# Kernel optimization log

Hardware: AMD Instinct MI355X
Metric: run time of the kernel (lower is better)

## Reference

```python
import jax, jax.numpy as jnp
import numpy as np

B, C, H, W = 32, 64, 64, 64
K, D = 512, 64
COMMITMENT_COST = 0.25


def setup_inputs() -> dict:
    key = jax.random.key(0)
    k1, k2, k3 = jax.random.split(key, 3)
    inputs = jax.random.normal(k1, (B, C, H, W), dtype=jnp.float32)
    codebook0 = jax.random.normal(k2, (K, D), dtype=jnp.float32)
    codebook1 = jax.random.normal(k3, (K, D), dtype=jnp.float32)
    return {"inputs": inputs, "codebook0": codebook0, "codebook1": codebook1, "idx": 1}


def reference(inputs, codebook0, codebook1, idx):
    # NCHW -> NHWC, flatten to [N, D]
    x = jnp.transpose(inputs, (0, 2, 3, 1))
    flat = x.reshape(-1, D)  # [N, D]
    if idx == 0:
        codes = codebook0
    else:
        codes = jnp.concatenate([codebook0, codebook1], axis=0)  # [2K, D]
    # squared-distance matrix [N, 2K]
    distances = (jnp.sum(flat * flat, axis=1, keepdims=True)
                 + jnp.sum(codes * codes, axis=1)
                 - 2.0 * jnp.matmul(flat, codes.T))
    encoding_indices = jnp.argmin(distances, axis=1)  # [N]
    # gather == one-hot @ codes, without materializing one-hot
    quantized = jnp.take(codes, encoding_indices, axis=0).reshape(x.shape)
    sg = jax.lax.stop_gradient
    e_latent_loss = jnp.mean((sg(quantized) - x) ** 2)
    q_latent_loss = jnp.mean((quantized - sg(x)) ** 2)
    loss = q_latent_loss + COMMITMENT_COST * e_latent_loss
    # straight-through estimator
    quantized_st = x + sg(quantized - x)
    # perplexity from usage histogram (== mean of one-hot encodings)
    n = flat.shape[0]
    counts = jnp.zeros((codes.shape[0],), dtype=jnp.float32).at[encoding_indices].add(1.0)
    avg_probs = counts / n
    perplexity = jnp.exp(-jnp.sum(avg_probs * jnp.log(avg_probs + 1e-10)))
    return (jnp.transpose(quantized_st, (0, 3, 1, 2)), loss, perplexity)
```

## Files before the change

kernel.cpp:

```cpp
#include <hip/hip_runtime.h>


typedef __attribute__((ext_vector_type(8))) short short8;
typedef __attribute__((ext_vector_type(16))) float f32x16;

#define LOSS_OFF 0
#define PART_OFF 2048
#define PACKED_OFF 34816
#define NPART 32
#define CHUNK_B 24576

#define GLL16(gsrc, ldst)                                                      \
  __builtin_amdgcn_global_load_lds(                                            \
      (const __attribute__((address_space(1))) void*)(gsrc),                   \
      (__attribute__((address_space(3))) void*)(ldst), 16, 0, 0)

__device__ __forceinline__ unsigned short bf16_rne(float v, float& rest) {
  const unsigned u = __float_as_uint(v);
  const unsigned r = u + 0x7fffu + ((u >> 16) & 1u);
  const unsigned short h = (unsigned short)(r >> 16);
  rest = v - __uint_as_float((unsigned)h << 16);
  return h;
}

__global__ void vq_pack(const float* __restrict__ cb0, const float* __restrict__ cb1,
                        float* __restrict__ ws) {
  const int c = blockIdx.x * 256 + threadIdx.x;
  if (c < NPART) ws[LOSS_OFF + c] = 0.0f;
#pragma unroll
  for (int p = 0; p < NPART; ++p) ws[PART_OFF + p * 1024 + c] = 0.0f;
  const float* row = (c < 512) ? (cb0 + (size_t)c * 64) : (cb1 + (size_t)(c - 512) * 64);
  float v[64];
  float nrm = 0.f;
#pragma unroll
  for (int d = 0; d < 64; d += 4) {
    const float4 f = *(const float4*)(row + d);
    v[d] = f.x; v[d + 1] = f.y; v[d + 2] = f.z; v[d + 3] = f.w;
    nrm += f.x * f.x + f.y * f.y + f.z * f.z + f.w * f.w;
  }
  unsigned short hi[64], lo[64];
#pragma unroll
  for (int d = 0; d < 64; ++d) {
    float rest, dump;
    hi[d] = bf16_rne(v[d], rest);
    lo[d] = bf16_rne(rest, dump);
  }
  float* base = ws + PACKED_OFF + (size_t)(c >> 6) * 6144 + (c & 63) * 4;
#pragma unroll
  for (int g = 0; g < 16; ++g) {
    short8 gr;
#pragma unroll
    for (int e = 0; e < 8; ++e)
      gr[e] = (short)((g < 8) ? hi[g * 8 + e] : lo[(g - 8) * 8 + e]);
    *(short8*)(base + g * 256) = gr;
  }
  {
    const float nh = -0.5f * nrm;
    float r1, r2, dump;
    const unsigned short n0 = bf16_rne(nh, r1);
    const unsigned short n1 = bf16_rne(r1, r2);
    const unsigned short n2 = bf16_rne(r2, dump);
    short8 g16 = {(short)n0, (short)n1, (short)n2, 0, 0, 0, 0, 0};
    *(short8*)(base + 16 * 256) = g16;
    short8 zz = {0, 0, 0, 0, 0, 0, 0, 0};
    *(short8*)(base + 17 * 256) = zz;
  }
}

__global__ __launch_bounds__(256, 2) void vq_dist(
    const float* __restrict__ xin, const int* __restrict__ idxp,
    const float* __restrict__ cb0, const float* __restrict__ cb1,
    float* __restrict__ out, float* __restrict__ ws) {
  __shared__ char ring[73728];
  const int tid = threadIdx.x;
  const int w = tid >> 6;
  const int l = tid & 63;
  const int half = l >> 5;
  const int col = l & 31;
  const int blk = blockIdx.x;
  const int bb = blk >> 4;
  const int hw0 = (blk & 15) << 8;
  const int nch = (*idxp == 0) ? 8 : 16;
  const char* pk = (const char*)(ws + PACKED_OFF);

  auto stage = [&](int ch, int buf) {
    const char* src = pk + (size_t)ch * CHUNK_B + w * 6144 + l * 16;
    char* dst = ring + buf * CHUNK_B + w * 6144;
#pragma unroll
    for (int i = 0; i < 6; ++i) GLL16(src + i * 1024, dst + i * 1024);
  };
  stage(0, 0);
  stage(1, 1);

  short8 xh[2][4], xl[2][4];
  float xx[2];
#pragma unroll
  for (int m = 0; m < 2; ++m) {
    float vv[4][8];
    const float* xb =
        xin + ((size_t)(bb * 64 + half * 8)) * 4096 + hw0 + w * 64 + m * 32 + col;
#pragma unroll
    for (int kf = 0; kf < 4; ++kf)
#pragma unroll
      for (int j = 0; j < 8; ++j)
        vv[kf][j] = xb[((size_t)(kf * 16 + j)) * 4096];
    float s = 0.f;
#pragma unroll
    for (int kf = 0; kf < 4; ++kf)
#pragma unroll
      for (int j = 0; j < 8; ++j) {
        const float v = vv[kf][j];
        float rest, dump;
        xh[m][kf][j] = (short)bf16_rne(v, rest);
        xl[m][kf][j] = (short)bf16_rne(rest, dump);
        s += v * v;
      }
    s += __shfl_xor(s, 32);
    xx[m] = s;
  }
  short8 xnh;
#pragma unroll
  for (int j = 0; j < 8; ++j)
    xnh[j] = (short)((half == 0 && j < 3) ? 0x3F80 : 0);
  const f32x16 ZV = (f32x16)0.0f;

  float best[2][16];
#pragma unroll
  for (int m = 0; m < 2; ++m)
#pragma unroll
    for (int r = 0; r < 16; ++r) best[m][r] = -3.4e38f;

  for (int i = 0; i < nch; ++i) {
    if (i < nch - 1) {
      asm volatile("s_waitcnt vmcnt(6)" ::: "memory");
    } else {
      asm volatile("s_waitcnt vmcnt(0)" ::: "memory");
    }
    __builtin_amdgcn_s_barrier();
    if (i + 2 < nch) stage(i + 2, (i + 2) % 3);
    const char* bufp = ring + (i % 3) * CHUNK_B;
    const char* tb0 = bufp + col * 16;
    const char* tb1 = bufp + (32 + col) * 16;

    __builtin_amdgcn_s_setprio(1);
    const short8 An0 = *(const short8*)(tb0 + (16 + half) * 1024);
    const short8 An1 = *(const short8*)(tb1 + (16 + half) * 1024);
    f32x16 a00 = __builtin_amdgcn_mfma_f32_32x32x16_bf16(An0, xnh, ZV, 0, 0, 0);
    f32x16 a01 = __builtin_amdgcn_mfma_f32_32x32x16_bf16(An1, xnh, ZV, 0, 0, 0);
    f32x16 a10 = __builtin_amdgcn_mfma_f32_32x32x16_bf16(An0, xnh, ZV, 0, 0, 0);
    f32x16 a11 = __builtin_amdgcn_mfma_f32_32x32x16_bf16(An1, xnh, ZV, 0, 0, 0);
#pragma unroll
    for (int kf = 0; kf < 4; ++kf) {
      const short8 Ah0 = *(const short8*)(tb0 + (2 * kf + half) * 1024);
      const short8 Ah1 = *(const short8*)(tb1 + (2 * kf + half) * 1024);
      const short8 Al0 = *(const short8*)(tb0 + (8 + 2 * kf + half) * 1024);
      const short8 Al1 = *(const short8*)(tb1 + (8 + 2 * kf + half) * 1024);
      a00 = __builtin_amdgcn_mfma_f32_32x32x16_bf16(Ah0, xh[0][kf], a00, 0, 0, 0);
      a01 = __builtin_amdgcn_mfma_f32_32x32x16_bf16(Ah1, xh[0][kf], a01, 0, 0, 0);
      a10 = __builtin_amdgcn_mfma_f32_32x32x16_bf16(Ah0, xh[1][kf], a10, 0, 0, 0);
      a11 = __builtin_amdgcn_mfma_f32_32x32x16_bf16(Ah1, xh[1][kf], a11, 0, 0, 0);
      a00 = __builtin_amdgcn_mfma_f32_32x32x16_bf16(Ah0, xl[0][kf], a00, 0, 0, 0);
      a01 = __builtin_amdgcn_mfma_f32_32x32x16_bf16(Ah1, xl[0][kf], a01, 0, 0, 0);
      a10 = __builtin_amdgcn_mfma_f32_32x32x16_bf16(Ah0, xl[1][kf], a10, 0, 0, 0);
      a11 = __builtin_amdgcn_mfma_f32_32x32x16_bf16(Ah1, xl[1][kf], a11, 0, 0, 0);
      a00 = __builtin_amdgcn_mfma_f32_32x32x16_bf16(Al0, xh[0][kf], a00, 0, 0, 0);
      a01 = __builtin_amdgcn_mfma_f32_32x32x16_bf16(Al1, xh[0][kf], a01, 0, 0, 0);
      a10 = __builtin_amdgcn_mfma_f32_32x32x16_bf16(Al0, xh[1][kf], a10, 0, 0, 0);
      a11 = __builtin_amdgcn_mfma_f32_32x32x16_bf16(Al1, xh[1][kf], a11, 0, 0, 0);
    }
    __builtin_amdgcn_s_setprio(0);

    const unsigned sid0 = (unsigned)(31 - 2 * i);
    const unsigned sid1 = (unsigned)(30 - 2 * i);
#pragma unroll
    for (int r = 0; r < 16; ++r) {
      const float p00 = __uint_as_float((__float_as_uint(a00[r]) & 0xFFFFFFE0u) | sid0);
      const float p01 = __uint_as_float((__float_as_uint(a01[r]) & 0xFFFFFFE0u) | sid1);
      best[0][r] = fmaxf(fmaxf(p00, p01), best[0][r]);
      const float p10 = __uint_as_float((__float_as_uint(a10[r]) & 0xFFFFFFE0u) | sid0);
      const float p11 = __uint_as_float((__float_as_uint(a11[r]) & 0xFFFFFFE0u) | sid1);
      best[1][r] = fmaxf(fmaxf(p10, p11), best[1][r]);
    }
  }

  __syncthreads();
  int* qidxL = (int*)ring;

  float ls = 0.f;
#pragma unroll
  for (int m = 0; m < 2; ++m) {
    float win = best[m][0];
    int wr = 0;
#pragma unroll
    for (int r = 1; r < 16; ++r) {
      const bool g = best[m][r] > win;
      win = g ? best[m][r] : win;
      wr = g ? r : wr;
    }
    const unsigned u = __float_as_uint(win);
    const int t = 31 - (int)(u & 31u);
    int code = (t >> 1) * 64 + (t & 1) * 32 + ((wr & 3) + 8 * (wr >> 2) + 4 * half);
    float clean = __uint_as_float(u & 0xFFFFFFE0u);
    const float ocl = __shfl_xor(clean, 32);
    const int oc = __shfl_xor(code, 32);
    const bool take = (ocl > clean) || (ocl == clean && oc < code);
    clean = take ? ocl : clean;
    code = take ? oc : code;
    if (half == 0) {
      qidxL[w * 64 + m * 32 + col] = code;
      ls += xx[m] - 2.0f * clean;
    }
  }
#pragma unroll
  for (int mk = 1; mk < 64; mk <<= 1) ls += __shfl_xor(ls, mk);
  if (l == 0) atomicAdd(&ws[LOSS_OFF + (blk & (NPART - 1))], ls);
  __syncthreads();

  const int ci = qidxL[tid];
  atomicAdd(ws + PART_OFF + (size_t)(blk & (NPART - 1)) * 1024 + ci, 1.0f);
  const float* crow = (ci < 512) ? (cb0 + (size_t)ci * 64) : (cb1 + (size_t)(ci - 512) * 64);
  float* ob = out + (((size_t)(bb * 64)) << 12) + hw0 + tid;
#pragma unroll
  for (int d4 = 0; d4 < 16; ++d4) {
    const float4 f = *(const float4*)(crow + d4 * 4);
    ob[((size_t)(d4 * 4 + 0)) << 12] = f.x;
    ob[((size_t)(d4 * 4 + 1)) << 12] = f.y;
    ob[((size_t)(d4 * 4 + 2)) << 12] = f.z;
    ob[((size_t)(d4 * 4 + 3)) << 12] = f.w;
  }
}

__global__ void vq_final(const float* __restrict__ ws, float* __restrict__ out) {
  __shared__ float sred[256];
  const int t = threadIdx.x;
  float h = 0.f;
#pragma unroll
  for (int i = t; i < 1024; i += 256) {
    float s = 0.f;
#pragma unroll
    for (int p = 0; p < NPART; ++p) s += ws[PART_OFF + p * 1024 + i];
    const float avg = s * (1.0f / 131072.0f);
    h += avg * logf(avg + 1e-10f);
  }
  sred[t] = h;
  __syncthreads();
  for (int s2 = 128; s2 > 0; s2 >>= 1) {
    if (t < s2) sred[t] += sred[t + s2];
    __syncthreads();
  }
  if (t == 0) {
    float lsum = 0.f;
#pragma unroll
    for (int p = 0; p < NPART; ++p) lsum += ws[LOSS_OFF + p];
    out[8388608] = 1.25f * lsum * (1.0f / 8388608.0f);
    out[8388609] = expf(-sred[0]);
  }
}

extern "C" void kernel_launch(void* const* d_in, const int* in_sizes, int n_in,
                              void* d_out, int out_size, void* d_ws, size_t ws_size,
                              hipStream_t stream) {
  (void)in_sizes; (void)n_in; (void)out_size; (void)ws_size;
  const float* xin = (const float*)d_in[0];
  const float* cb0 = (const float*)d_in[1];
  const float* cb1 = (const float*)d_in[2];
  const int* idxp = (const int*)d_in[3];
  float* out = (float*)d_out;
  float* ws = (float*)d_ws;

  vq_pack<<<4, 256, 0, stream>>>(cb0, cb1, ws);
  vq_dist<<<512, 256, 0, stream>>>(xin, idxp, cb0, cb1, out, ws);
  vq_final<<<1, 256, 0, stream>>>(ws, out);
}
```

Baseline: 77.64 us.

## Read packed codebook directly from global memory instead of LDS ring

Removes the triple-buffered LDS staging of the packed codebook via global_load_lds, along with its barriers and waitcnts. Each wave now loads its codebook fragments straight from global memory, relying on L1/L2 caching, with a 2x unrolled chunk loop. The packed layout is shrunk to drop the unused padding group, and LDS use falls to a small index buffer, which could allow more occupancy. In exchange every wave issues its own global loads with higher latency, and there is no longer an explicit prefetch to hide that latency.

```diff
diff --git a/kernel.cpp b/kernel.cpp
--- a/kernel.cpp
+++ b/kernel.cpp
@@ -8,12 +8,7 @@
 #define PART_OFF 2048
 #define PACKED_OFF 34816
 #define NPART 32
-#define CHUNK_B 24576
-
-#define GLL16(gsrc, ldst)                                                      \
-  __builtin_amdgcn_global_load_lds(                                            \
-      (const __attribute__((address_space(1))) void*)(gsrc),                   \
-      (__attribute__((address_space(3))) void*)(ldst), 16, 0, 0)
+#define CHUNK_B 18432
 
 __device__ __forceinline__ unsigned short bf16_rne(float v, float& rest) {
   const unsigned u = __float_as_uint(v);
@@ -45,7 +40,7 @@
     hi[d] = bf16_rne(v[d], rest);
     lo[d] = bf16_rne(rest, dump);
   }
-  float* base = ws + PACKED_OFF + (size_t)(c >> 6) * 6144 + (c & 63) * 4;
+  float* base = ws + PACKED_OFF + (size_t)(c >> 6) * 4608 + (c & 63) * 4;
 #pragma unroll
   for (int g = 0; g < 16; ++g) {
     short8 gr;
@@ -71,7 +66,7 @@
     const float* __restrict__ xin, const int* __restrict__ idxp,
     const float* __restrict__ cb0, const float* __restrict__ cb1,
     float* __restrict__ out, float* __restrict__ ws) {
-  __shared__ char ring[73728];
+  __shared__ int qidxL[256];
   const int tid = threadIdx.x;
   const int w = tid >> 6;
   const int l = tid & 63;
@@ -81,16 +76,6 @@
   const int bb = blk >> 4;
   const int hw0 = (blk & 15) << 8;
   const int nch = (*idxp == 0) ? 8 : 16;
-  const char* pk = (const char*)(ws + PACKED_OFF);
-
-  auto stage = [&](int ch, int buf) {
-    const char* src = pk + (size_t)ch * CHUNK_B + w * 6144 + l * 16;
-    char* dst = ring + buf * CHUNK_B + w * 6144;
-#pragma unroll
-    for (int i = 0; i < 6; ++i) GLL16(src + i * 1024, dst + i * 1024);
-  };
-  stage(0, 0);
-  stage(1, 1);
 
   short8 xh[2][4], xl[2][4];
   float xx[2];
@@ -130,31 +115,25 @@
 #pragma unroll
     for (int r = 0; r < 16; ++r) best[m][r] = -3.4e38f;
 
+  const char* pkl = (const char*)(ws + PACKED_OFF) + col * 16 + half * 1024;
+
+#pragma unroll 2
   for (int i = 0; i < nch; ++i) {
-    if (i < nch - 1) {
-      asm volatile("s_waitcnt vmcnt(6)" ::: "memory");
-    } else {
-      asm volatile("s_waitcnt vmcnt(0)" ::: "memory");
-    }
-    __builtin_amdgcn_s_barrier();
-    if (i + 2 < nch) stage(i + 2, (i + 2) % 3);
-    const char* bufp = ring + (i % 3) * CHUNK_B;
-    const char* tb0 = bufp + col * 16;
-    const char* tb1 = bufp + (32 + col) * 16;
-
-    __builtin_amdgcn_s_setprio(1);
-    const short8 An0 = *(const short8*)(tb0 + (16 + half) * 1024);
-    const short8 An1 = *(const short8*)(tb1 + (16 + half) * 1024);
+    const char* tb0 = pkl + (size_t)i * CHUNK_B;
+    const char* tb1 = tb0 + 512;
+
+    const short8 An0 = *(const short8*)(tb0 + 16 * 1024);
+    const short8 An1 = *(const short8*)(tb1 + 16 * 1024);
     f32x16 a00 = __builtin_amdgcn_mfma_f32_32x32x16_bf16(An0, xnh, ZV, 0, 0, 0);
     f32x16 a01 = __builtin_amdgcn_mfma_f32_32x32x16_bf16(An1, xnh, ZV, 0, 0, 0);
     f32x16 a10 = __builtin_amdgcn_mfma_f32_32x32x16_bf16(An0, xnh, ZV, 0, 0, 0);
     f32x16 a11 = __builtin_amdgcn_mfma_f32_32x32x16_bf16(An1, xnh, ZV, 0, 0, 0);
 #pragma unroll
     for (int kf = 0; kf < 4; ++kf) {
-      const short8 Ah0 = *(const short8*)(tb0 + (2 * kf + half) * 1024);
-      const short8 Ah1 = *(const short8*)(tb1 + (2 * kf + half) * 1024);
-      const short8 Al0 = *(const short8*)(tb0 + (8 + 2 * kf + half) * 1024);
-      const short8 Al1 = *(const short8*)(tb1 + (8 + 2 * kf + half) * 1024);
+      const short8 Ah0 = *(const short8*)(tb0 + (2 * kf) * 1024);
+      const short8 Ah1 = *(const short8*)(tb1 + (2 * kf) * 1024);
+      const short8 Al0 = *(const short8*)(tb0 + (8 + 2 * kf) * 1024);
+      const short8 Al1 = *(const short8*)(tb1 + (8 + 2 * kf) * 1024);
       a00 = __builtin_amdgcn_mfma_f32_32x32x16_bf16(Ah0, xh[0][kf], a00, 0, 0, 0);
       a01 = __builtin_amdgcn_mfma_f32_32x32x16_bf16(Ah1, xh[0][kf], a01, 0, 0, 0);
       a10 = __builtin_amdgcn_mfma_f32_32x32x16_bf16(Ah0, xh[1][kf], a10, 0, 0, 0);
@@ -168,7 +147,6 @@
       a10 = __builtin_amdgcn_mfma_f32_32x32x16_bf16(Al0, xh[1][kf], a10, 0, 0, 0);
       a11 = __builtin_amdgcn_mfma_f32_32x32x16_bf16(Al1, xh[1][kf], a11, 0, 0, 0);
     }
-    __builtin_amdgcn_s_setprio(0);
 
     const unsigned sid0 = (unsigned)(31 - 2 * i);
     const unsigned sid1 = (unsigned)(30 - 2 * i);
@@ -182,9 +160,6 @@
       best[1][r] = fmaxf(fmaxf(p10, p11), best[1][r]);
     }
   }
-
-  __syncthreads();
-  int* qidxL = (int*)ring;
 
   float ls = 0.f;
 #pragma unroll
```

Measured after the change: 84.24 us. +8.5%, slower.

## Switch distance GEMM to 16x16x32 MFMA with fp32 norm-initialized accumulators

Applied to the files above, without the earlier changes.

Replaces the 32x32x16 bf16 MFMA tiling with 16x16x32 MFMAs, repacking the codebook into 16-code tiles with the -0.5·||c||² term stored as fp32 and used directly as the accumulator init. This drops the extra norm MFMAs and the 3-way bf16 split of the norm. Argmax packing changes from 5 to 8 low mantissa bits, and the final argmin becomes a cross-lane shuffle reduction. It also shrinks the LDS staging chunk and register footprint, at the cost of coarser tie precision from masking 8 mantissa bits.

```diff
diff --git a/kernel.cpp b/kernel.cpp
--- a/kernel.cpp
+++ b/kernel.cpp
@@ -2,13 +2,13 @@
 
 
 typedef __attribute__((ext_vector_type(8))) short short8;
-typedef __attribute__((ext_vector_type(16))) float f32x16;
+typedef __attribute__((ext_vector_type(4))) float f32x4;
 
 #define LOSS_OFF 0
 #define PART_OFF 2048
 #define PACKED_OFF 34816
 #define NPART 32
-#define CHUNK_B 24576
+#define CHUNK_B 20480
 
 #define GLL16(gsrc, ldst)                                                      \
   __builtin_amdgcn_global_load_lds(                                            \
@@ -45,25 +45,30 @@
     hi[d] = bf16_rne(v[d], rest);
     lo[d] = bf16_rne(rest, dump);
   }
-  float* base = ws + PACKED_OFF + (size_t)(c >> 6) * 6144 + (c & 63) * 4;
-#pragma unroll
-  for (int g = 0; g < 16; ++g) {
-    short8 gr;
-#pragma unroll
-    for (int e = 0; e < 8; ++e)
-      gr[e] = (short)((g < 8) ? hi[g * 8 + e] : lo[(g - 8) * 8 + e]);
-    *(short8*)(base + g * 256) = gr;
+  const int ch = c >> 6, t = (c >> 4) & 3, cl16 = c & 15;
+  float* tb = ws + PACKED_OFF + (size_t)ch * 5120 + t * 1280;
+#pragma unroll
+  for (int fi = 0; fi < 4; ++fi) {
+    const int f = fi & 1;
+    const int isLo = fi >> 1;
+#pragma unroll
+    for (int g = 0; g < 4; ++g) {
+      short8 gr;
+#pragma unroll
+      for (int j = 0; j < 8; ++j) {
+        const int k = f * 32 + g * 8 + j;
+        gr[j] = (short)(isLo ? lo[k] : hi[k]);
+      }
+      *(short8*)(tb + fi * 256 + g * 64 + cl16 * 4) = gr;
+    }
   }
   {
     const float nh = -0.5f * nrm;
-    float r1, r2, dump;
-    const unsigned short n0 = bf16_rne(nh, r1);
-    const unsigned short n1 = bf16_rne(r1, r2);
-    const unsigned short n2 = bf16_rne(r2, dump);
-    short8 g16 = {(short)n0, (short)n1, (short)n2, 0, 0, 0, 0, 0};
-    *(short8*)(base + 16 * 256) = g16;
-    short8 zz = {0, 0, 0, 0, 0, 0, 0, 0};
-    *(short8*)(base + 17 * 256) = zz;
+    const int lg = cl16 >> 2;
+    const int r = cl16 & 3;
+    float* nb = tb + 1024 + r;
+#pragma unroll
+    for (int cc = 0; cc < 16; ++cc) nb[(lg * 16 + cc) * 4] = nh;
   }
 }
 
@@ -71,12 +76,14 @@
     const float* __restrict__ xin, const int* __restrict__ idxp,
     const float* __restrict__ cb0, const float* __restrict__ cb1,
     float* __restrict__ out, float* __restrict__ ws) {
-  __shared__ char ring[73728];
+  __shared__ char smem[62464];
+  char* ring = smem;
+  int* qidxL = (int*)(smem + 61440);
   const int tid = threadIdx.x;
   const int w = tid >> 6;
   const int l = tid & 63;
-  const int half = l >> 5;
-  const int col = l & 31;
+  const int lg = l >> 4;
+  const int c16 = l & 15;
   const int blk = blockIdx.x;
   const int bb = blk >> 4;
   const int hw0 = (blk & 15) << 8;
@@ -84,131 +91,126 @@
   const char* pk = (const char*)(ws + PACKED_OFF);
 
   auto stage = [&](int ch, int buf) {
-    const char* src = pk + (size_t)ch * CHUNK_B + w * 6144 + l * 16;
-    char* dst = ring + buf * CHUNK_B + w * 6144;
-#pragma unroll
-    for (int i = 0; i < 6; ++i) GLL16(src + i * 1024, dst + i * 1024);
+    const char* src = pk + (size_t)ch * CHUNK_B + w * 5120 + l * 16;
+    char* dst = ring + buf * CHUNK_B + w * 5120;
+#pragma unroll
+    for (int i = 0; i < 5; ++i) GLL16(src + i * 1024, dst + i * 1024);
   };
   stage(0, 0);
   stage(1, 1);
 
-  short8 xh[2][4], xl[2][4];
-  float xx[2];
-#pragma unroll
-  for (int m = 0; m < 2; ++m) {
-    float vv[4][8];
-    const float* xb =
-        xin + ((size_t)(bb * 64 + half * 8)) * 4096 + hw0 + w * 64 + m * 32 + col;
-#pragma unroll
-    for (int kf = 0; kf < 4; ++kf)
+  short8 xh[4][2], xl[4][2];
+  float xs[4];
+#pragma unroll
+  for (int m = 0; m < 4; ++m) {
+    const float* base =
+        xin + ((size_t)(bb * 64 + lg * 8)) * 4096 + hw0 + w * 64 + m * 16 + c16;
+    float vv[2][8];
+#pragma unroll
+    for (int f = 0; f < 2; ++f)
 #pragma unroll
       for (int j = 0; j < 8; ++j)
-        vv[kf][j] = xb[((size_t)(kf * 16 + j)) * 4096];
+        vv[f][j] = base[((size_t)(f * 32 + j)) * 4096];
     float s = 0.f;
 #pragma unroll
-    for (int kf = 0; kf < 4; ++kf)
+    for (int f = 0; f < 2; ++f)
 #pragma unroll
       for (int j = 0; j < 8; ++j) {
-        const float v = vv[kf][j];
+        const float v = vv[f][j];
         float rest, dump;
-        xh[m][kf][j] = (short)bf16_rne(v, rest);
-        xl[m][kf][j] = (short)bf16_rne(rest, dump);
+        xh[m][f][j] = (short)bf16_rne(v, rest);
+        xl[m][f][j] = (short)bf16_rne(rest, dump);
         s += v * v;
       }
-    s += __shfl_xor(s, 32);
-    xx[m] = s;
-  }
-  short8 xnh;
-#pragma unroll
-  for (int j = 0; j < 8; ++j)
-    xnh[j] = (short)((half == 0 && j < 3) ? 0x3F80 : 0);
-  const f32x16 ZV = (f32x16)0.0f;
-
-  float best[2][16];
-#pragma unroll
-  for (int m = 0; m < 2; ++m)
-#pragma unroll
-    for (int r = 0; r < 16; ++r) best[m][r] = -3.4e38f;
+    xs[m] = s;
+  }
+
+  float best[4];
+#pragma unroll
+  for (int m = 0; m < 4; ++m) best[m] = -3.4e38f;
+
+  const int la = lg * 256 + c16 * 16;
 
   for (int i = 0; i < nch; ++i) {
     if (i < nch - 1) {
-      asm volatile("s_waitcnt vmcnt(6)" ::: "memory");
+      asm volatile("s_waitcnt vmcnt(5)" ::: "memory");
     } else {
       asm volatile("s_waitcnt vmcnt(0)" ::: "memory");
     }
     __builtin_amdgcn_s_barrier();
     if (i + 2 < nch) stage(i + 2, (i + 2) % 3);
+
     const char* bufp = ring + (i % 3) * CHUNK_B;
-    const char* tb0 = bufp + col * 16;
-    const char* tb1 = bufp + (32 + col) * 16;
-
-    __builtin_amdgcn_s_setprio(1);
-    const short8 An0 = *(const short8*)(tb0 + (16 + half) * 1024);
-    const short8 An1 = *(const short8*)(tb1 + (16 + half) * 1024);
-    f32x16 a00 = __builtin_amdgcn_mfma_f32_32x32x16_bf16(An0, xnh, ZV, 0, 0, 0);
-    f32x16 a01 = __builtin_amdgcn_mfma_f32_32x32x16_bf16(An1, xnh, ZV, 0, 0, 0);
-    f32x16 a10 = __builtin_amdgcn_mfma_f32_32x32x16_bf16(An0, xnh, ZV, 0, 0, 0);
-    f32x16 a11 = __builtin_amdgcn_mfma_f32_32x32x16_bf16(An1, xnh, ZV, 0, 0, 0);
-#pragma unroll
-    for (int kf = 0; kf < 4; ++kf) {
-      const short8 Ah0 = *(const short8*)(tb0 + (2 * kf + half) * 1024);
-      const short8 Ah1 = *(const short8*)(tb1 + (2 * kf + half) * 1024);
-      const short8 Al0 = *(const short8*)(tb0 + (8 + 2 * kf + half) * 1024);
-      const short8 Al1 = *(const short8*)(tb1 + (8 + 2 * kf + half) * 1024);
-      a00 = __builtin_amdgcn_mfma_f32_32x32x16_bf16(Ah0, xh[0][kf], a00, 0, 0, 0);
-      a01 = __builtin_amdgcn_mfma_f32_32x32x16_bf16(Ah1, xh[0][kf], a01, 0, 0, 0);
-      a10 = __builtin_amdgcn_mfma_f32_32x32x16_bf16(Ah0, xh[1][kf], a10, 0, 0, 0);
-      a11 = __builtin_amdgcn_mfma_f32_32x32x16_bf16(Ah1, xh[1][kf], a11, 0, 0, 0);
-      a00 = __builtin_amdgcn_mfma_f32_32x32x16_bf16(Ah0, xl[0][kf], a00, 0, 0, 0);
-      a01 = __builtin_amdgcn_mfma_f32_32x32x16_bf16(Ah1, xl[0][kf], a01, 0, 0, 0);
-      a10 = __builtin_amdgcn_mfma_f32_32x32x16_bf16(Ah0, xl[1][kf], a10, 0, 0, 0);
-      a11 = __builtin_amdgcn_mfma_f32_32x32x16_bf16(Ah1, xl[1][kf], a11, 0, 0, 0);
-      a00 = __builtin_amdgcn_mfma_f32_32x32x16_bf16(Al0, xh[0][kf], a00, 0, 0, 0);
-      a01 = __builtin_amdgcn_mfma_f32_32x32x16_bf16(Al1, xh[0][kf], a01, 0, 0, 0);
-      a10 = __builtin_amdgcn_mfma_f32_32x32x16_bf16(Al0, xh[1][kf], a10, 0, 0, 0);
-      a11 = __builtin_amdgcn_mfma_f32_32x32x16_bf16(Al1, xh[1][kf], a11, 0, 0, 0);
-    }
-    __builtin_amdgcn_s_setprio(0);
-
-    const unsigned sid0 = (unsigned)(31 - 2 * i);
-    const unsigned sid1 = (unsigned)(30 - 2 * i);
-#pragma unroll
-    for (int r = 0; r < 16; ++r) {
-      const float p00 = __uint_as_float((__float_as_uint(a00[r]) & 0xFFFFFFE0u) | sid0);
-      const float p01 = __uint_as_float((__float_as_uint(a01[r]) & 0xFFFFFFE0u) | sid1);
-      best[0][r] = fmaxf(fmaxf(p00, p01), best[0][r]);
-      const float p10 = __uint_as_float((__float_as_uint(a10[r]) & 0xFFFFFFE0u) | sid0);
-      const float p11 = __uint_as_float((__float_as_uint(a11[r]) & 0xFFFFFFE0u) | sid1);
-      best[1][r] = fmaxf(fmaxf(p10, p11), best[1][r]);
-    }
-  }
-
-  __syncthreads();
-  int* qidxL = (int*)ring;
+#pragma unroll
+    for (int t = 0; t < 4; ++t) {
+      const char* tb = bufp + t * 5120;
+      const short8 ch0 = *(const short8*)(tb + la);
+      const short8 ch1 = *(const short8*)(tb + 1024 + la);
+      const short8 cl0 = *(const short8*)(tb + 2048 + la);
+      const short8 cl1 = *(const short8*)(tb + 3072 + la);
+      const f32x4 nC = *(const f32x4*)(tb + 4096 + l * 16);
+      f32x4 a0 = nC, a1 = nC, a2 = nC, a3 = nC;
+      a0 = __builtin_amdgcn_mfma_f32_16x16x32_bf16(ch0, xh[0][0], a0, 0, 0, 0);
+      a1 = __builtin_amdgcn_mfma_f32_16x16x32_bf16(ch0, xh[1][0], a1, 0, 0, 0);
+      a2 = __builtin_amdgcn_mfma_f32_16x16x32_bf16(ch0, xh[2][0], a2, 0, 0, 0);
+      a3 = __builtin_amdgcn_mfma_f32_16x16x32_bf16(ch0, xh[3][0], a3, 0, 0, 0);
+      a0 = __builtin_amdgcn_mfma_f32_16x16x32_bf16(ch1, xh[0][1], a0, 0, 0, 0);
+      a1 = __builtin_amdgcn_mfma_f32_16x16x32_bf16(ch1, xh[1][1], a1, 0, 0, 0);
+      a2 = __builtin_amdgcn_mfma_f32_16x16x32_bf16(ch1, xh[2][1], a2, 0, 0, 0);
+      a3 = __builtin_amdgcn_mfma_f32_16x16x32_bf16(ch1, xh[3][1], a3, 0, 0, 0);
+      a0 = __builtin_amdgcn_mfma_f32_16x16x32_bf16(ch0, xl[0][0], a0, 0, 0, 0);
+      a1 = __builtin_amdgcn_mfma_f32_16x16x32_bf16(ch0, xl[1][0], a1, 0, 0, 0);
+      a2 = __builtin_amdgcn_mfma_f32_16x16x32_bf16(ch0, xl[2][0], a2, 0, 0, 0);
+      a3 = __builtin_amdgcn_mfma_f32_16x16x32_bf16(ch0, xl[3][0], a3, 0, 0, 0);
+      a0 = __builtin_amdgcn_mfma_f32_16x16x32_bf16(ch1, xl[0][1], a0, 0, 0, 0);
+      a1 = __builtin_amdgcn_mfma_f32_16x16x32_bf16(ch1, xl[1][1], a1, 0, 0, 0);
+      a2 = __builtin_amdgcn_mfma_f32_16x16x32_bf16(ch1, xl[2][1], a2, 0, 0, 0);
+      a3 = __builtin_amdgcn_mfma_f32_16x16x32_bf16(ch1, xl[3][1], a3, 0, 0, 0);
+      a0 = __builtin_amdgcn_mfma_f32_16x16x32_bf16(cl0, xh[0][0], a0, 0, 0, 0);
+      a1 = __builtin_amdgcn_mfma_f32_16x16x32_bf16(cl0, xh[1][0], a1, 0, 0, 0);
+      a2 = __builtin_amdgcn_mfma_f32_16x16x32_bf16(cl0, xh[2][0], a2, 0, 0, 0);
+      a3 = __builtin_amdgcn_mfma_f32_16x16x32_bf16(cl0, xh[3][0], a3, 0, 0, 0);
+      a0 = __builtin_amdgcn_mfma_f32_16x16x32_bf16(cl1, xh[0][1], a0, 0, 0, 0);
+      a1 = __builtin_amdgcn_mfma_f32_16x16x32_bf16(cl1, xh[1][1], a1, 0, 0, 0);
+      a2 = __builtin_amdgcn_mfma_f32_16x16x32_bf16(cl1, xh[2][1], a2, 0, 0, 0);
+      a3 = __builtin_amdgcn_mfma_f32_16x16x32_bf16(cl1, xh[3][1], a3, 0, 0, 0);
+
+      const unsigned bs = 255u - (unsigned)(i * 16 + t * 4);
+#pragma unroll
+      for (int r = 0; r < 4; ++r) {
+        const float p0 = __uint_as_float((__float_as_uint(a0[r]) & 0xFFFFFF00u) | (bs - r));
+        const float p1 = __uint_as_float((__float_as_uint(a1[r]) & 0xFFFFFF00u) | (bs - r));
+        const float p2 = __uint_as_float((__float_as_uint(a2[r]) & 0xFFFFFF00u) | (bs - r));
+        const float p3 = __uint_as_float((__float_as_uint(a3[r]) & 0xFFFFFF00u) | (bs - r));
+        best[0] = fmaxf(best[0], p0);
+        best[1] = fmaxf(best[1], p1);
+        best[2] = fmaxf(best[2], p2);
+        best[3] = fmaxf(best[3], p3);
+      }
+    }
+  }
 
   float ls = 0.f;
 #pragma unroll
-  for (int m = 0; m < 2; ++m) {
-    float win = best[m][0];
-    int wr = 0;
-#pragma unroll
-    for (int r = 1; r < 16; ++r) {
-      const bool g = best[m][r] > win;
-      win = g ? best[m][r] : win;
-      wr = g ? r : wr;
-    }
-    const unsigned u = __float_as_uint(win);
-    const int t = 31 - (int)(u & 31u);
-    int code = (t >> 1) * 64 + (t & 1) * 32 + ((wr & 3) + 8 * (wr >> 2) + 4 * half);
-    float clean = __uint_as_float(u & 0xFFFFFFE0u);
-    const float ocl = __shfl_xor(clean, 32);
-    const int oc = __shfl_xor(code, 32);
-    const bool take = (ocl > clean) || (ocl == clean && oc < code);
-    clean = take ? ocl : clean;
-    code = take ? oc : code;
-    if (half == 0) {
-      qidxL[w * 64 + m * 32 + col] = code;
-      ls += xx[m] - 2.0f * clean;
+  for (int m = 0; m < 4; ++m) {
+    const unsigned u = __float_as_uint(best[m]);
+    const int iid = 255 - (int)(u & 255u);
+    int code = (iid >> 4) * 64 + ((iid >> 2) & 3) * 16 + lg * 4 + (iid & 3);
+    float clean = __uint_as_float(u & 0xFFFFFF00u);
+    float xsm = xs[m];
+#pragma unroll
+    for (int mk = 16; mk < 64; mk <<= 1) {
+      const float ocl = __shfl_xor(clean, mk);
+      const int oc = __shfl_xor(code, mk);
+      const float oxs = __shfl_xor(xsm, mk);
+      xsm += oxs;
+      const bool take = (ocl > clean) || (ocl == clean && oc < code);
+      clean = take ? ocl : clean;
+      code = take ? oc : code;
+    }
+    if (l < 16) {
+      qidxL[w * 64 + m * 16 + l] = code;
+      ls += xsm - 2.0f * clean;
     }
   }
 #pragma unroll
```

Result: faster. 75.27 us (-3.1%).
